# Performance work log

Measured on AMD Instinct MI355X. Metric: run time of the kernel, lower is better.

The kernel has to match this reference:

```python
import jax, jax.numpy as jnp
import numpy as np

TOP_K = 2  # config.moe_config.top_k


def setup_inputs() -> dict:
    key = jax.random.key(0)
    k0, k1, k2, k3 = jax.random.split(key, 4)
    T, H, I, E = 8192, 2048, 1408, 8  # tokens, hidden, moe_intermediate, experts
    x = jax.random.normal(k0, (T, H), jnp.float32)
    router_weight = jax.random.normal(k1, (E, H), jnp.float32) * 0.02
    gate_up_proj = jax.random.normal(k2, (E, H, 2 * I), jnp.float32) * 0.02
    down_proj = jax.random.normal(k3, (E, I, H), jnp.float32) * 0.02
    return {"x": x, "router_weight": router_weight,
            "gate_up_proj": gate_up_proj, "down_proj": down_proj}


def _moe_forward(x, router_weight, gate_up_proj, down_proj):
    # Router: fp32 gating linear (no bias), softmax over experts, top-k,
    # then scatter the top-k softmax weights into a dense [T, E] gate tensor
    # (topk_version=False path of Router.top_k_softmax).
    T = x.shape[0]
    E = router_weight.shape[0]
    logits = x.astype(jnp.float32) @ router_weight.T            # [T, E]
    probs = jax.nn.softmax(logits, axis=-1)                      # [T, E]
    topk_w, topk_idx = jax.lax.top_k(probs, TOP_K)               # [T, k]
    gates = jnp.zeros_like(logits).at[
        jnp.arange(T)[:, None], topk_idx].set(topk_w)            # [T, E] sparse gates

    # Grouped expert MLP (GroupedMLP): merged gate/up GEMM, SwiGLU, down GEMM.
    # Dispatch/permute + grouped GEMM + weighted combine is mathematically
    # out[t] = sum_e gates[t, e] * MLP_e(x[t]); expressed here as a fixed loop
    # over the small expert set with masked accumulation (jit-friendly).
    out = jnp.zeros_like(x)
    for e in range(E):
        gu = x @ gate_up_proj[e]                                 # [T, 2I]
        g, u = jnp.split(gu, 2, axis=-1)
        h = (jax.nn.silu(g) * u) @ down_proj[e]                  # [T, H]
        out = out + gates[:, e:e + 1].astype(x.dtype) * h
    return out


def reference(x, router_weight, gate_up_proj, down_proj):
    return _moe_forward(x, router_weight, gate_up_proj, down_proj)
```

## Files before the change

kernel.cpp:

```cpp
#include <hip/hip_runtime.h>
#include <hip/hip_bf16.h>
#include <cstdint>
#include <cstddef>

#define T_TOK 8192
#define H_DIM 2048
#define I_DIM 1408
#define E_NUM 8
#define BM 128
#define BK 64
#define ROWS_CAP (2 * T_TOK + E_NUM * BM)
#define MAX_MT (ROWS_CAP / BM)
#define NT1 (I_DIM / 64)
#define NT2 (H_DIM / 128)

typedef __attribute__((ext_vector_type(8))) short short8;
typedef __attribute__((ext_vector_type(4))) float f32x4;
typedef __attribute__((ext_vector_type(8))) unsigned short bf16x8;
typedef __attribute__((ext_vector_type(4))) unsigned short bf16x4;
typedef __attribute__((ext_vector_type(8))) _Float16 h16x8;

static __device__ __forceinline__ unsigned short f2bf(float f) {
  unsigned u = __float_as_uint(f);
  u += 0x7FFFu + ((u >> 16) & 1u);
  return (unsigned short)(u >> 16);
}

static __device__ __forceinline__ void gld_lds16(const void* g, void* l) {
  __builtin_amdgcn_global_load_lds(
      (__attribute__((address_space(1))) unsigned int*)g,
      (__attribute__((address_space(3))) unsigned int*)l, 16, 0, 0);
}

template <int G>
static __device__ __forceinline__ void remap_tile(int bid, int nb, int nt_cols,
                                                  int& m_t, int& n_t) {
  int chunk = nb >> 3;
  int wg = (bid & 7) * chunk + (bid >> 3);
  int grp = wg / (nt_cols * G);
  int rem = wg % (nt_cols * G);
  n_t = rem / G;
  m_t = grp * G + rem % G;
}

__global__ __launch_bounds__(256) void router_kernel(
    const float* __restrict__ x, const float* __restrict__ rw,
    unsigned short* __restrict__ xb,
    int* __restrict__ topk_idx, float* __restrict__ topk_w, int* __restrict__ meta) {
  int t = blockIdx.x * 4 + (threadIdx.x >> 6);
  int lane = threadIdx.x & 63;
  const float* xr = x + (size_t)t * H_DIM;
  unsigned short* xbr = xb + (size_t)t * H_DIM;
  float acc[E_NUM];
#pragma unroll
  for (int e = 0; e < E_NUM; e++) acc[e] = 0.f;
  for (int j = lane * 4; j < H_DIM; j += 256) {
    f32x4 v = *(const f32x4*)(xr + j);
    bf16x4 b;
#pragma unroll
    for (int u = 0; u < 4; u++) b[u] = f2bf(v[u]);
    *(bf16x4*)(xbr + j) = b;
#pragma unroll
    for (int e = 0; e < E_NUM; e++) {
      f32x4 w = *(const f32x4*)(rw + e * H_DIM + j);
      acc[e] += v[0] * w[0] + v[1] * w[1] + v[2] * w[2] + v[3] * w[3];
    }
  }
#pragma unroll
  for (int e = 0; e < E_NUM; e++) {
    float v = acc[e];
#pragma unroll
    for (int s = 32; s > 0; s >>= 1) v += __shfl_xor(v, s);
    acc[e] = v;
  }
  if (lane == 0) {
    int i0 = 0;
#pragma unroll
    for (int e = 1; e < E_NUM; e++) if (acc[e] > acc[i0]) i0 = e;
    int i1 = (i0 == 0) ? 1 : 0;
#pragma unroll
    for (int e = 0; e < E_NUM; e++) if (e != i0 && acc[e] > acc[i1]) i1 = e;
    float mx = acc[0];
#pragma unroll
    for (int e = 1; e < E_NUM; e++) mx = fmaxf(mx, acc[e]);
    float sum = 0.f, p[E_NUM];
#pragma unroll
    for (int e = 0; e < E_NUM; e++) { p[e] = expf(acc[e] - mx); sum += p[e]; }
    float inv = 1.f / sum;
    topk_idx[t * 2] = i0;  topk_idx[t * 2 + 1] = i1;
    topk_w[t * 2] = p[i0] * inv;  topk_w[t * 2 + 1] = p[i1] * inv;
    atomicAdd(&meta[i0], 1);
    atomicAdd(&meta[i1], 1);
  }
}

__global__ void scan_kernel(int* __restrict__ meta, int* __restrict__ row_token) {
  __shared__ int s_off[E_NUM + 1];
  if (threadIdx.x == 0) {
    int o = 0, nt = 0;
    for (int e = 0; e < E_NUM; e++) {
      meta[16 + e] = o; s_off[e] = o;
      int c = meta[e];
      int mtc = (c + BM - 1) / BM;
      for (int m = 0; m < mtc; m++) { meta[64 + nt] = e; meta[256 + nt] = o + m * BM; nt++; }
      o += mtc * BM;
      meta[8 + e] = 0;
    }
    meta[16 + E_NUM] = o; s_off[E_NUM] = o;
    meta[32] = nt;
  }
  __syncthreads();
  for (int e = 0; e < E_NUM; e++) {
    int lo = s_off[e] + meta[e], hi = s_off[e + 1];
    for (int r = lo + (int)threadIdx.x; r < hi; r += 64) row_token[r] = -1;
  }
}

__global__ __launch_bounds__(256) void bucket_kernel(
    const int* __restrict__ topk_idx, int* __restrict__ meta,
    int* __restrict__ row_token, int* __restrict__ tok2row) {
  int i = blockIdx.x * 256 + threadIdx.x;
  if (i >= 2 * T_TOK) return;
  int e = topk_idx[i];
  int pos = atomicAdd(&meta[8 + e], 1);
  int r = meta[16 + e] + pos;
  row_token[r] = i >> 1;
  tok2row[i] = r;
}

__global__ __launch_bounds__(256) void tcvt2_kernel(
    const float* __restrict__ wgu, const float* __restrict__ wdn,
    unsigned short* __restrict__ wgu_t, unsigned short* __restrict__ wd_t) {
  __shared__ unsigned short st[64 * 64];
  int z = blockIdx.z;
  const float* src; unsigned short* dst; int R, C;
  if (z < E_NUM) {
    R = H_DIM; C = 2 * I_DIM;
    src = wgu + (size_t)z * R * C;  dst = wgu_t + (size_t)z * R * C;
  } else {
    R = I_DIM; C = H_DIM;
    src = wdn + (size_t)(z - E_NUM) * R * C;  dst = wd_t + (size_t)(z - E_NUM) * R * C;
  }
  int c0 = blockIdx.x * 64, r0 = blockIdx.y * 64;
  if (c0 >= C || r0 >= R) return;
  int tid = threadIdx.x;
  int q = tid & 15, s = tid >> 4;
#pragma unroll
  for (int it = 0; it < 4; it++) {
    int rr = it * 16 + s;
    f32x4 v = *(const f32x4*)(src + (size_t)(r0 + rr) * C + c0 + q * 4);
    int cr = rr >> 3, w = rr & 7;
#pragma unroll
    for (int j = 0; j < 4; j++) {
      int c = q * 4 + j;
      st[c * 64 + ((cr ^ (q & 7)) << 3) + w] = f2bf(v[j]);
    }
  }
  __syncthreads();
  int cc = tid >> 3, ca = tid & 7;
#pragma unroll
  for (int it = 0; it < 2; it++) {
    int c = it * 32 + cc;
    bf16x8 v = *(const bf16x8*)(st + c * 64 + ((ca ^ ((c >> 2) & 7)) << 3));
    *(bf16x8*)(dst + (size_t)(c0 + c) * R + r0 + ca * 8) = v;
  }
}

__global__ __launch_bounds__(256) void gemm1_kernel(
    const unsigned short* __restrict__ xb,
    const unsigned short* __restrict__ wgu,
    unsigned short* __restrict__ hbuf,
    const int* __restrict__ row_token, const int* __restrict__ meta) {
  int m_t, n_t;
  remap_tile<4>(blockIdx.x, NT1 * MAX_MT, NT1, m_t, n_t);
  if (m_t >= meta[32]) return;
  int e = meta[64 + m_t];
  int row0 = meta[256 + m_t];
  int n0h = n_t * 64;

  __shared__ alignas(16) char smem[65536];

  int tid = threadIdx.x, lane = tid & 63, wid = tid >> 6;
  const unsigned short* asrc[4];
  const unsigned short* bsrc[4];
  {
    const unsigned short* wb = wgu + (size_t)e * (2 * (size_t)I_DIM) * H_DIM;
#pragma unroll
    for (int i = 0; i < 4; i++) {
      int r = i * 32 + (tid >> 3);
      int ch = ((tid & 7) ^ (r & 7)) * 8;
      int tok = row_token[row0 + r];
      if (tok < 0) tok = 0;
      asrc[i] = xb + (size_t)tok * H_DIM + ch;
      int wr = (r < 64) ? (n0h + r) : (I_DIM + n0h + (r - 64));
      bsrc[i] = wb + (size_t)wr * H_DIM + ch;
    }
  }
  f32x4 acc[4][4] = {};
  int mrow = (wid >> 1) * 64 + (lane & 15);
  int brow = (wid & 1) * 64 + (lane & 15);

#define STAGE1(buf, kof_)                                                     \
  {                                                                           \
    int kof = (kof_);                                                         \
    char* b = smem + (buf) * 32768;                                           \
    _Pragma("unroll") for (int i = 0; i < 4; i++) {                           \
      gld_lds16(asrc[i] + kof, b + i * 4096 + wid * 1024);                    \
      gld_lds16(bsrc[i] + kof, b + 16384 + i * 4096 + wid * 1024);            \
    }                                                                         \
  }

  constexpr int NK1 = H_DIM / BK;
  STAGE1(0, 0);
  STAGE1(1, BK);
  for (int kt = 0; kt < NK1; kt++) {
    int cur = kt & 1;
    if (kt + 1 < NK1) { asm volatile("s_waitcnt vmcnt(8)" ::: "memory"); }
    else              { asm volatile("s_waitcnt vmcnt(0)" ::: "memory"); }
    __builtin_amdgcn_s_barrier();
    const unsigned short* sA = (const unsigned short*)(smem + cur * 32768);
    const unsigned short* sB = sA + 8192;
#pragma unroll
    for (int kk = 0; kk < 2; kk++) {
      int krd = ((kk * 4 + (lane >> 4)) ^ (lane & 7)) * 8;
      short8 af[4], bf[4];
#pragma unroll
      for (int f = 0; f < 4; f++) {
        af[f] = *(const short8*)(sA + (mrow + f * 16) * BK + krd);
        bf[f] = *(const short8*)(sB + (brow + f * 16) * BK + krd);
      }
#pragma unroll
      for (int fm = 0; fm < 4; fm++)
#pragma unroll
        for (int fn = 0; fn < 4; fn++)
          acc[fm][fn] = __builtin_amdgcn_mfma_f32_16x16x32_bf16(af[fm], bf[fn], acc[fm][fn], 0, 0, 0);
    }
    asm volatile("" ::: "memory");
    __builtin_amdgcn_s_barrier();
    asm volatile("" ::: "memory");
    if (kt + 2 < NK1) STAGE1(cur, (kt + 2) * BK);
  }

  float* xw = (float*)smem + (wid >> 1) * 4096;
  if (wid & 1) {
#pragma unroll
    for (int fm = 0; fm < 4; fm++)
#pragma unroll
      for (int r = 0; r < 4; r++) {
        int mloc = fm * 16 + (lane >> 4) * 4 + r;
#pragma unroll
        for (int fn = 0; fn < 4; fn++)
          xw[mloc * 64 + fn * 16 + (lane & 15)] = acc[fm][fn][r];
      }
  }
  __syncthreads();
  if (!(wid & 1)) {
    int mbase = row0 + (wid >> 1) * 64;
#pragma unroll
    for (int fm = 0; fm < 4; fm++)
#pragma unroll
      for (int r = 0; r < 4; r++) {
        int mloc = fm * 16 + (lane >> 4) * 4 + r;
        size_t rbase = (size_t)(mbase + mloc) * I_DIM + n0h;
#pragma unroll
        for (int fn = 0; fn < 4; fn++) {
          float g = acc[fm][fn][r];
          float u = xw[mloc * 64 + fn * 16 + (lane & 15)];
          float hv = (g / (1.f + __expf(-g))) * u;
          hbuf[rbase + fn * 16 + (lane & 15)] = f2bf(hv);
        }
      }
  }
}

__global__ __launch_bounds__(256) void gemm2_kernel(
    const unsigned short* __restrict__ hbuf,
    const unsigned short* __restrict__ wd,
    _Float16* __restrict__ part,
    const int* __restrict__ meta) {
  int m_t, n_t;
  remap_tile<8>(blockIdx.x, NT2 * MAX_MT, NT2, m_t, n_t);
  if (m_t >= meta[32]) return;
  int e = meta[64 + m_t];
  int row0 = meta[256 + m_t];
  int n0 = n_t * 128;

  __shared__ alignas(16) char smem[65536];

  int tid = threadIdx.x, lane = tid & 63, wid = tid >> 6;
  const unsigned short* asrc[4];
  const unsigned short* bsrc[4];
  {
    const unsigned short* wb = wd + (size_t)e * (size_t)H_DIM * I_DIM;
#pragma unroll
    for (int i = 0; i < 4; i++) {
      int r = i * 32 + (tid >> 3);
      int ch = ((tid & 7) ^ (r & 7)) * 8;
      asrc[i] = hbuf + (size_t)(row0 + r) * I_DIM + ch;
      bsrc[i] = wb + (size_t)(n0 + r) * I_DIM + ch;
    }
  }
  f32x4 acc[4][4] = {};
  int mrow = (wid >> 1) * 64 + (lane & 15);
  int brow = (wid & 1) * 64 + (lane & 15);

  constexpr int NK2 = I_DIM / BK;
  STAGE1(0, 0);
  STAGE1(1, BK);
  for (int kt = 0; kt < NK2; kt++) {
    int cur = kt & 1;
    if (kt + 1 < NK2) { asm volatile("s_waitcnt vmcnt(8)" ::: "memory"); }
    else              { asm volatile("s_waitcnt vmcnt(0)" ::: "memory"); }
    __builtin_amdgcn_s_barrier();
    const unsigned short* sA = (const unsigned short*)(smem + cur * 32768);
    const unsigned short* sB = sA + 8192;
#pragma unroll
    for (int kk = 0; kk < 2; kk++) {
      int krd = ((kk * 4 + (lane >> 4)) ^ (lane & 7)) * 8;
      short8 af[4], bf[4];
#pragma unroll
      for (int f = 0; f < 4; f++) {
        af[f] = *(const short8*)(sA + (mrow + f * 16) * BK + krd);
        bf[f] = *(const short8*)(sB + (brow + f * 16) * BK + krd);
      }
#pragma unroll
      for (int fm = 0; fm < 4; fm++)
#pragma unroll
        for (int fn = 0; fn < 4; fn++)
          acc[fm][fn] = __builtin_amdgcn_mfma_f32_16x16x32_bf16(af[fm], bf[fn], acc[fm][fn], 0, 0, 0);
    }
    asm volatile("" ::: "memory");
    __builtin_amdgcn_s_barrier();
    asm volatile("" ::: "memory");
    if (kt + 2 < NK2) STAGE1(cur, (kt + 2) * BK);
  }
  _Float16* stg = (_Float16*)(smem + wid * 8192);
  int l15 = lane & 15;
#pragma unroll
  for (int fm = 0; fm < 4; fm++)
#pragma unroll
    for (int r = 0; r < 4; r++) {
      int mloc = fm * 16 + (lane >> 4) * 4 + r;
#pragma unroll
      for (int fn = 0; fn < 4; fn++) {
        int nl = fn * 16 + l15;
        stg[mloc * 64 + (((nl >> 3) ^ (mloc & 7)) << 3) + (nl & 7)] =
            (_Float16)acc[fm][fn][r];
      }
    }
  int m0 = (wid >> 1) * 64;
  int nbase = n0 + (wid & 1) * 64;
  int ca = lane & 7;
#pragma unroll
  for (int it = 0; it < 8; it++) {
    int mr = it * 8 + (lane >> 3);
    h16x8 v = *(const h16x8*)(stg + mr * 64 + ((ca ^ (mr & 7)) << 3));
    *(h16x8*)(part + (size_t)(row0 + m0 + mr) * H_DIM + nbase + ca * 8) = v;
  }
}

__global__ __launch_bounds__(256) void combine_kernel(
    const _Float16* __restrict__ part, const int* __restrict__ tok2row,
    const float* __restrict__ topk_w, float* __restrict__ out) {
  int t = blockIdx.x;
  int c = threadIdx.x * 8;
  int r0 = tok2row[2 * t], r1 = tok2row[2 * t + 1];
  float w0 = topk_w[2 * t], w1 = topk_w[2 * t + 1];
  h16x8 p0 = *(const h16x8*)(part + (size_t)r0 * H_DIM + c);
  h16x8 p1 = *(const h16x8*)(part + (size_t)r1 * H_DIM + c);
  float* o = out + (size_t)t * H_DIM + c;
  f32x4 lo, hi;
#pragma unroll
  for (int j = 0; j < 4; j++) lo[j] = w0 * (float)p0[j] + w1 * (float)p1[j];
#pragma unroll
  for (int j = 0; j < 4; j++) hi[j] = w0 * (float)p0[4 + j] + w1 * (float)p1[4 + j];
  *(f32x4*)o = lo;
  *(f32x4*)(o + 4) = hi;
}

extern "C" void kernel_launch(void* const* d_in, const int* in_sizes, int n_in,
                              void* d_out, int out_size, void* d_ws, size_t ws_size,
                              hipStream_t stream) {
  const float* x   = (const float*)d_in[0];
  const float* rw  = (const float*)d_in[1];
  const float* wgu = (const float*)d_in[2];
  const float* wdn = (const float*)d_in[3];
  float* out = (float*)d_out;

  char* ws = (char*)d_ws;
  size_t off = 0;
  auto alloc = [&](size_t bytes) {
    void* p = ws + off;
    off += (bytes + 255) & ~(size_t)255;
    return p;
  };
  int* meta            = (int*)alloc(4096);
  int* topk_idx        = (int*)alloc((size_t)2 * T_TOK * 4);
  float* topk_w        = (float*)alloc((size_t)2 * T_TOK * 4);
  int* tok2row         = (int*)alloc((size_t)2 * T_TOK * 4);
  int* row_token       = (int*)alloc((size_t)ROWS_CAP * 4);
  unsigned short* xb    = (unsigned short*)alloc((size_t)T_TOK * H_DIM * 2);
  unsigned short* wgu_t = (unsigned short*)alloc((size_t)E_NUM * 2 * I_DIM * H_DIM * 2);
  unsigned short* wd_t  = (unsigned short*)alloc((size_t)E_NUM * H_DIM * I_DIM * 2);
  unsigned short* hbuf  = (unsigned short*)alloc((size_t)ROWS_CAP * I_DIM * 2);
  _Float16* part = (_Float16*)wgu_t;

  if (off > ws_size) {
    (void)hipMemsetAsync(d_out, 0, (size_t)out_size * sizeof(float), stream);
    return;
  }

  (void)hipMemsetAsync(meta, 0, 4096, stream);

  tcvt2_kernel<<<dim3(2 * I_DIM / 64, H_DIM / 64, 2 * E_NUM), 256, 0, stream>>>(wgu, wdn, wgu_t, wd_t);

  router_kernel<<<T_TOK / 4, 256, 0, stream>>>(x, rw, xb, topk_idx, topk_w, meta);
  scan_kernel<<<1, 64, 0, stream>>>(meta, row_token);
  bucket_kernel<<<(2 * T_TOK + 255) / 256, 256, 0, stream>>>(topk_idx, meta, row_token, tok2row);

  gemm1_kernel<<<NT1 * MAX_MT, 256, 0, stream>>>(xb, wgu_t, hbuf, row_token, meta);
  gemm2_kernel<<<NT2 * MAX_MT, 256, 0, stream>>>(hbuf, wd_t, part, meta);
  combine_kernel<<<T_TOK, 256, 0, stream>>>(part, tok2row, topk_w, out);
}
```

Baseline: 718.4 us.

## Fuse fp32 weight conversion into GEMM B-tile loads, drop transpose pre-pass

Removes the separate kernel that converts and transposes both expert weight tensors to bf16 every call. Each GEMM now reads fp32 weights straight from global memory into registers, converts them to bf16, and writes them transposed and swizzled into LDS. The pipeline gains extra vmcnt/lgkmcnt waits and barriers. Each weight tile is now re-read in fp32 by every M tile, so weight traffic doubles per load and repeats across M tiles, and the register staging adds VGPR pressure.

```diff
diff --git a/kernel.cpp b/kernel.cpp
--- a/kernel.cpp
+++ b/kernel.cpp
@@ -16,6 +16,7 @@
 
 typedef __attribute__((ext_vector_type(8))) short short8;
 typedef __attribute__((ext_vector_type(4))) float f32x4;
+typedef __attribute__((ext_vector_type(2))) float f32x2;
 typedef __attribute__((ext_vector_type(8))) unsigned short bf16x8;
 typedef __attribute__((ext_vector_type(4))) unsigned short bf16x4;
 typedef __attribute__((ext_vector_type(8))) _Float16 h16x8;
@@ -128,47 +129,17 @@
   tok2row[i] = r;
 }
 
-__global__ __launch_bounds__(256) void tcvt2_kernel(
-    const float* __restrict__ wgu, const float* __restrict__ wdn,
-    unsigned short* __restrict__ wgu_t, unsigned short* __restrict__ wd_t) {
-  __shared__ unsigned short st[64 * 64];
-  int z = blockIdx.z;
-  const float* src; unsigned short* dst; int R, C;
-  if (z < E_NUM) {
-    R = H_DIM; C = 2 * I_DIM;
-    src = wgu + (size_t)z * R * C;  dst = wgu_t + (size_t)z * R * C;
-  } else {
-    R = I_DIM; C = H_DIM;
-    src = wdn + (size_t)(z - E_NUM) * R * C;  dst = wd_t + (size_t)(z - E_NUM) * R * C;
-  }
-  int c0 = blockIdx.x * 64, r0 = blockIdx.y * 64;
-  if (c0 >= C || r0 >= R) return;
-  int tid = threadIdx.x;
-  int q = tid & 15, s = tid >> 4;
-#pragma unroll
-  for (int it = 0; it < 4; it++) {
-    int rr = it * 16 + s;
-    f32x4 v = *(const f32x4*)(src + (size_t)(r0 + rr) * C + c0 + q * 4);
-    int cr = rr >> 3, w = rr & 7;
-#pragma unroll
-    for (int j = 0; j < 4; j++) {
-      int c = q * 4 + j;
-      st[c * 64 + ((cr ^ (q & 7)) << 3) + w] = f2bf(v[j]);
-    }
-  }
-  __syncthreads();
-  int cc = tid >> 3, ca = tid & 7;
-#pragma unroll
-  for (int it = 0; it < 2; it++) {
-    int c = it * 32 + cc;
-    bf16x8 v = *(const bf16x8*)(st + c * 64 + ((ca ^ ((c >> 2) & 7)) << 3));
-    *(bf16x8*)(dst + (size_t)(c0 + c) * R + r0 + ca * 8) = v;
-  }
-}
+#define STAGE_A(buf, kof_)                                                    \
+  {                                                                           \
+    int kof = (kof_);                                                         \
+    char* b = smem + (buf) * 32768;                                           \
+    _Pragma("unroll") for (int i = 0; i < 4; i++)                             \
+      gld_lds16(asrc[i] + kof, b + i * 4096 + wid * 1024);                    \
+  }
 
 __global__ __launch_bounds__(256) void gemm1_kernel(
     const unsigned short* __restrict__ xb,
-    const unsigned short* __restrict__ wgu,
+    const float* __restrict__ wgu,
     unsigned short* __restrict__ hbuf,
     const int* __restrict__ row_token, const int* __restrict__ meta) {
   int m_t, n_t;
@@ -177,14 +148,13 @@
   int e = meta[64 + m_t];
   int row0 = meta[256 + m_t];
   int n0h = n_t * 64;
+  constexpr int CB = 2 * I_DIM;
 
   __shared__ alignas(16) char smem[65536];
 
   int tid = threadIdx.x, lane = tid & 63, wid = tid >> 6;
   const unsigned short* asrc[4];
-  const unsigned short* bsrc[4];
   {
-    const unsigned short* wb = wgu + (size_t)e * (2 * (size_t)I_DIM) * H_DIM;
 #pragma unroll
     for (int i = 0; i < 4; i++) {
       int r = i * 32 + (tid >> 3);
@@ -192,32 +162,63 @@
       int tok = row_token[row0 + r];
       if (tok < 0) tok = 0;
       asrc[i] = xb + (size_t)tok * H_DIM + ch;
-      int wr = (r < 64) ? (n0h + r) : (I_DIM + n0h + (r - 64));
-      bsrc[i] = wb + (size_t)wr * H_DIM + ch;
-    }
-  }
+    }
+  }
+  const float* bcol[2];
+  int npair = tid & 63, kc0 = tid >> 6;
+  {
+    const float* wb = wgu + (size_t)e * H_DIM * CB;
+    int n = npair * 2;
+    int col = (n < 64) ? (n0h + n) : (I_DIM + n0h + (n - 64));
+#pragma unroll
+    for (int u = 0; u < 2; u++)
+      bcol[u] = wb + (size_t)((kc0 + u * 4) * 8) * CB + col;
+  }
+  f32x2 rB[2][8];
+  auto loadB = [&](int kof) {
+#pragma unroll
+    for (int u = 0; u < 2; u++)
+#pragma unroll
+      for (int j = 0; j < 8; j++)
+        rB[u][j] = *(const f32x2*)(bcol[u] + (size_t)(kof + j) * CB);
+  };
+  auto writeB = [&](int buf) {
+    unsigned short* sBw = (unsigned short*)(smem + buf * 32768 + 16384);
+#pragma unroll
+    for (int u = 0; u < 2; u++) {
+      int kchunk = kc0 + u * 4;
+#pragma unroll
+      for (int o = 0; o < 2; o++) {
+        int n = npair * 2 + o;
+        bf16x8 v;
+#pragma unroll
+        for (int j = 0; j < 8; j++) v[j] = f2bf(rB[u][j][o]);
+        *(bf16x8*)(sBw + n * 64 + ((kchunk ^ (n & 7)) << 3)) = v;
+      }
+    }
+  };
+
   f32x4 acc[4][4] = {};
   int mrow = (wid >> 1) * 64 + (lane & 15);
   int brow = (wid & 1) * 64 + (lane & 15);
 
-#define STAGE1(buf, kof_)                                                     \
-  {                                                                           \
-    int kof = (kof_);                                                         \
-    char* b = smem + (buf) * 32768;                                           \
-    _Pragma("unroll") for (int i = 0; i < 4; i++) {                           \
-      gld_lds16(asrc[i] + kof, b + i * 4096 + wid * 1024);                    \
-      gld_lds16(bsrc[i] + kof, b + 16384 + i * 4096 + wid * 1024);            \
-    }                                                                         \
-  }
-
-  constexpr int NK1 = H_DIM / BK;
-  STAGE1(0, 0);
-  STAGE1(1, BK);
-  for (int kt = 0; kt < NK1; kt++) {
-    int cur = kt & 1;
-    if (kt + 1 < NK1) { asm volatile("s_waitcnt vmcnt(8)" ::: "memory"); }
-    else              { asm volatile("s_waitcnt vmcnt(0)" ::: "memory"); }
-    __builtin_amdgcn_s_barrier();
+  constexpr int NK = H_DIM / BK;
+  loadB(0);
+  STAGE_A(0, 0);
+  asm volatile("s_waitcnt vmcnt(0)" ::: "memory");
+  writeB(0);
+  loadB(BK);
+  STAGE_A(1, BK);
+  asm volatile("s_waitcnt vmcnt(0)" ::: "memory");
+  writeB(1);
+  asm volatile("s_waitcnt lgkmcnt(0)" ::: "memory");
+  __builtin_amdgcn_s_barrier();
+  int cur = 0;
+  for (int kt = 0; kt < NK; kt++) {
+    if (kt + 2 < NK) {
+      loadB((kt + 2) * BK);
+      __builtin_amdgcn_sched_barrier(0);
+    }
     const unsigned short* sA = (const unsigned short*)(smem + cur * 32768);
     const unsigned short* sB = sA + 8192;
 #pragma unroll
@@ -237,8 +238,14 @@
     }
     asm volatile("" ::: "memory");
     __builtin_amdgcn_s_barrier();
-    asm volatile("" ::: "memory");
-    if (kt + 2 < NK1) STAGE1(cur, (kt + 2) * BK);
+    asm volatile("s_waitcnt vmcnt(0)" ::: "memory");
+    if (kt + 2 < NK) {
+      writeB(cur);
+      STAGE_A(cur, (kt + 2) * BK);
+    }
+    asm volatile("s_waitcnt lgkmcnt(0)" ::: "memory");
+    __builtin_amdgcn_s_barrier();
+    cur ^= 1;
   }
 
   float* xw = (float*)smem + (wid >> 1) * 4096;
@@ -275,7 +282,7 @@
 
 __global__ __launch_bounds__(256) void gemm2_kernel(
     const unsigned short* __restrict__ hbuf,
-    const unsigned short* __restrict__ wd,
+    const float* __restrict__ wdn,
     _Float16* __restrict__ part,
     const int* __restrict__ meta) {
   int m_t, n_t;
@@ -284,34 +291,74 @@
   int e = meta[64 + m_t];
   int row0 = meta[256 + m_t];
   int n0 = n_t * 128;
+  constexpr int CB = H_DIM;
 
   __shared__ alignas(16) char smem[65536];
 
   int tid = threadIdx.x, lane = tid & 63, wid = tid >> 6;
   const unsigned short* asrc[4];
-  const unsigned short* bsrc[4];
   {
-    const unsigned short* wb = wd + (size_t)e * (size_t)H_DIM * I_DIM;
 #pragma unroll
     for (int i = 0; i < 4; i++) {
       int r = i * 32 + (tid >> 3);
       int ch = ((tid & 7) ^ (r & 7)) * 8;
       asrc[i] = hbuf + (size_t)(row0 + r) * I_DIM + ch;
-      bsrc[i] = wb + (size_t)(n0 + r) * I_DIM + ch;
-    }
-  }
+    }
+  }
+  const float* bcol[2];
+  int npair = tid & 63, kc0 = tid >> 6;
+  {
+    const float* wb = wdn + (size_t)e * I_DIM * CB;
+    int col = n0 + npair * 2;
+#pragma unroll
+    for (int u = 0; u < 2; u++)
+      bcol[u] = wb + (size_t)((kc0 + u * 4) * 8) * CB + col;
+  }
+  f32x2 rB[2][8];
+  auto loadB = [&](int kof) {
+#pragma unroll
+    for (int u = 0; u < 2; u++)
+#pragma unroll
+      for (int j = 0; j < 8; j++)
+        rB[u][j] = *(const f32x2*)(bcol[u] + (size_t)(kof + j) * CB);
+  };
+  auto writeB = [&](int buf) {
+    unsigned short* sBw = (unsigned short*)(smem + buf * 32768 + 16384);
+#pragma unroll
+    for (int u = 0; u < 2; u++) {
+      int kchunk = kc0 + u * 4;
+#pragma unroll
+      for (int o = 0; o < 2; o++) {
+        int n = npair * 2 + o;
+        bf16x8 v;
+#pragma unroll
+        for (int j = 0; j < 8; j++) v[j] = f2bf(rB[u][j][o]);
+        *(bf16x8*)(sBw + n * 64 + ((kchunk ^ (n & 7)) << 3)) = v;
+      }
+    }
+  };
+
   f32x4 acc[4][4] = {};
   int mrow = (wid >> 1) * 64 + (lane & 15);
   int brow = (wid & 1) * 64 + (lane & 15);
 
-  constexpr int NK2 = I_DIM / BK;
-  STAGE1(0, 0);
-  STAGE1(1, BK);
-  for (int kt = 0; kt < NK2; kt++) {
-    int cur = kt & 1;
-    if (kt + 1 < NK2) { asm volatile("s_waitcnt vmcnt(8)" ::: "memory"); }
-    else              { asm volatile("s_waitcnt vmcnt(0)" ::: "memory"); }
-    __builtin_amdgcn_s_barrier();
+  constexpr int NK = I_DIM / BK;
+  loadB(0);
+  STAGE_A(0, 0);
+  asm volatile("s_waitcnt vmcnt(0)" ::: "memory");
+  writeB(0);
+  loadB(BK);
+  STAGE_A(1, BK);
+  asm volatile("s_waitcnt vmcnt(0)" ::: "memory");
+  writeB(1);
+  asm volatile("s_waitcnt lgkmcnt(0)" ::: "memory");
+  __builtin_amdgcn_s_barrier();
+  int cur = 0;
+  for (int kt = 0; kt < NK; kt++) {
+    if (kt + 2 < NK) {
+      loadB((kt + 2) * BK);
+      __builtin_amdgcn_sched_barrier(0);
+    }
     const unsigned short* sA = (const unsigned short*)(smem + cur * 32768);
     const unsigned short* sB = sA + 8192;
 #pragma unroll
@@ -331,8 +378,14 @@
     }
     asm volatile("" ::: "memory");
     __builtin_amdgcn_s_barrier();
-    asm volatile("" ::: "memory");
-    if (kt + 2 < NK2) STAGE1(cur, (kt + 2) * BK);
+    asm volatile("s_waitcnt vmcnt(0)" ::: "memory");
+    if (kt + 2 < NK) {
+      writeB(cur);
+      STAGE_A(cur, (kt + 2) * BK);
+    }
+    asm volatile("s_waitcnt lgkmcnt(0)" ::: "memory");
+    __builtin_amdgcn_s_barrier();
+    cur ^= 1;
   }
   _Float16* stg = (_Float16*)(smem + wid * 8192);
   int l15 = lane & 15;
@@ -400,10 +453,8 @@
   int* tok2row         = (int*)alloc((size_t)2 * T_TOK * 4);
   int* row_token       = (int*)alloc((size_t)ROWS_CAP * 4);
   unsigned short* xb    = (unsigned short*)alloc((size_t)T_TOK * H_DIM * 2);
-  unsigned short* wgu_t = (unsigned short*)alloc((size_t)E_NUM * 2 * I_DIM * H_DIM * 2);
-  unsigned short* wd_t  = (unsigned short*)alloc((size_t)E_NUM * H_DIM * I_DIM * 2);
   unsigned short* hbuf  = (unsigned short*)alloc((size_t)ROWS_CAP * I_DIM * 2);
-  _Float16* part = (_Float16*)wgu_t;
+  _Float16* part        = (_Float16*)alloc((size_t)ROWS_CAP * H_DIM * 2);
 
   if (off > ws_size) {
     (void)hipMemsetAsync(d_out, 0, (size_t)out_size * sizeof(float), stream);
@@ -412,13 +463,11 @@
 
   (void)hipMemsetAsync(meta, 0, 4096, stream);
 
-  tcvt2_kernel<<<dim3(2 * I_DIM / 64, H_DIM / 64, 2 * E_NUM), 256, 0, stream>>>(wgu, wdn, wgu_t, wd_t);
-
   router_kernel<<<T_TOK / 4, 256, 0, stream>>>(x, rw, xb, topk_idx, topk_w, meta);
   scan_kernel<<<1, 64, 0, stream>>>(meta, row_token);
   bucket_kernel<<<(2 * T_TOK + 255) / 256, 256, 0, stream>>>(topk_idx, meta, row_token, tok2row);
 
-  gemm1_kernel<<<NT1 * MAX_MT, 256, 0, stream>>>(xb, wgu_t, hbuf, row_token, meta);
-  gemm2_kernel<<<NT2 * MAX_MT, 256, 0, stream>>>(hbuf, wd_t, part, meta);
+  gemm1_kernel<<<NT1 * MAX_MT, 256, 0, stream>>>(xb, wgu, hbuf, row_token, meta);
+  gemm2_kernel<<<NT2 * MAX_MT, 256, 0, stream>>>(hbuf, wdn, part, meta);
   combine_kernel<<<T_TOK, 256, 0, stream>>>(part, tok2row, topk_w, out);
 }
```

Measured after the change: 828.4 us. 1.15x slower.
